# Kernel tuning notes

Measured on AMD Instinct MI355X. Metric: run time of the kernel, lower is better.

The kernel has to match this reference:

```python
import jax, jax.numpy as jnp
import numpy as np

R = 40            # guided-filter radius (81x81 window)
EPS = 1e-3
BETA = 2.996 / 300.0  # visibility_m = 300.0


def _box_sum(x, r=R):
    """Zero-padded sliding-window sum over an (B,C,H,W) tensor.
    Matches F.avg_pool2d(x, 2r+1, stride=1, padding=r) * (2r+1)^2
    (count_include_pad=True), computed in O(HW) via prefix sums."""
    B, C, H, W = x.shape

    def _along(y, axis, L):
        cs = jnp.cumsum(y, axis=axis)
        pad = [(0, 0)] * 4
        pad[axis] = (1, 0)
        cs = jnp.pad(cs, pad)  # cs[i] = sum of first i elements
        hi = jnp.clip(jnp.arange(L) + r + 1, 0, L)
        lo = jnp.clip(jnp.arange(L) - r, 0, L)
        return jnp.take(cs, hi, axis=axis) - jnp.take(cs, lo, axis=axis)

    x = _along(x, 2, H)
    x = _along(x, 3, W)
    return x


def _guided_filter(I, p, r=R, eps=EPS):
    N = (2 * r + 1) ** 2
    mean_I = _box_sum(I, r) / N
    mean_p = _box_sum(p, r) / N
    mean_Ip = _box_sum(I * p, r) / N
    cov_Ip = mean_Ip - mean_I * mean_p
    mean_II = _box_sum(I * I, r) / N
    var_I = mean_II - mean_I * mean_I
    a = cov_Ip / (var_I + eps)
    b = mean_p - a * mean_I
    mean_a = _box_sum(a, r) / N
    mean_b = _box_sum(b, r) / N
    return mean_a * I + mean_b


def setup_inputs() -> dict:
    key = jax.random.key(0)
    k1, k2 = jax.random.split(key)
    B, H, W = 8, 768, 1280
    img = jax.random.uniform(k1, (B, 3, H, W), dtype=jnp.float32)
    depth = jax.random.uniform(k2, (B, 1, H, W), dtype=jnp.float32) * 500.0
    return {"img": img, "depth": depth}


def reference(img, depth):
    B, _, H, W = img.shape
    t_raw = jnp.clip(jnp.exp(-BETA * depth), 0.0, 1.0)          # (B,1,H,W)
    gray = (0.299 * img[:, 0:1] + 0.587 * img[:, 1:2]
            + 0.114 * img[:, 2:3])                               # (B,1,H,W)
    t = _guided_filter(gray, t_raw)                               # (B,1,H,W)

    # atmospheric light A: mean color over the k farthest pixels, per image
    k = max(10, int(0.001 * H * W))
    k = min(k, H * W)
    depth_flat = depth.reshape(B, -1)                             # (B,HW)
    img_flat = img.reshape(B, 3, -1)                              # (B,3,HW)
    _, idx = jax.lax.top_k(depth_flat, k)                         # (B,k)
    A = jnp.take_along_axis(img_flat, idx[:, None, :], axis=2).mean(axis=2)
    A = A.reshape(B, 3, 1, 1)

    return img * t + A * (1.0 - t)
```

## Files before the change

kernel.cpp:

```cpp
#include <hip/hip_runtime.h>
#include <hip/hip_fp16.h>
#include <stdint.h>

typedef unsigned int u32;

#define Bn 8
#define Hn 768
#define Wn 1280
#define HWs (Hn*Wn)
#define Rr 40
#define NNinv (1.0f/6561.0f)
#define KTOP 983
#define BETA_C (2.996f/300.0f)
#define EQCAP 4096
#define TK_BPI 480
#define NCH 96
#define SEGV 16
#define NSEGV 48
#define HIMG 4
#define TK1_WAVES 16
#define TW 640
#define CW 680

#define OFF_F     0
#define OFF_AB1   (16*HWs)
#define OFF_AB2   (24*HWs)
#define OFF_CS4f  (32*HWs)
#define OFF_CS2f  (36*HWs)
#define OFF_TAILf (38*HWs)

#define OFFH_FOVF 0
#define OFFH_AB   (4*HWs)
#define CS_N      (HIMG*NCH*Wn)
#define OFFH_CS4  (12*HWs)
#define OFFH_CS2  (OFFH_CS4 + 4*CS_N)
#define OFFH_TAIL (OFFH_CS2 + 2*CS_N)

__device__ __forceinline__ float4 f4add(float4 a, float4 b){ return make_float4(a.x+b.x,a.y+b.y,a.z+b.z,a.w+b.w); }
__device__ __forceinline__ float4 f4sub(float4 a, float4 b){ return make_float4(a.x-b.x,a.y-b.y,a.z-b.z,a.w-b.w); }

__device__ __forceinline__ u32 h2_to_u32(__half2 h){ union { __half2 h; u32 u; } c; c.h = h; return c.u; }
__device__ __forceinline__ __half2 u32_to_h2(u32 u){ union { u32 u; __half2 h; } c; c.u = u; return c.h; }


__global__ __launch_bounds__(256) void gA_kernel(const float* __restrict__ img, const float* __restrict__ depth,
    uint2* __restrict__ F, float4* __restrict__ CS4){
  __shared__ float4 lds[769];
  __shared__ float4 wtot[4];
  int blk = blockIdx.x;
  int xt = blk & 1;
  int t2 = blk >> 1;
  int b = t2 / NCH, ch = t2 % NCH;
  int x0 = xt*TW;
  int cstart = xt ? (TW - Rr) : 0;
  int tid = threadIdx.x;
  int lane = tid & 63, wv = tid >> 6;
  float4 acc[3];
  #pragma unroll
  for (int j = 0; j < 3; ++j) acc[j] = make_float4(0,0,0,0);
  for (int r = 0; r < 8; ++r){
    int y = ch*8 + r;
    const float* ir = img + ((size_t)(b*3+0)*Hn + y)*Wn + cstart;
    const float* ig = img + ((size_t)(b*3+1)*Hn + y)*Wn + cstart;
    const float* ib = img + ((size_t)(b*3+2)*Hn + y)*Wn + cstart;
    const float* dp = depth + ((size_t)b*Hn + y)*Wn + cstart;
    __syncthreads();
    for (int i = tid; i < 768; i += 256){
      if (i < CW){
        float rr = ir[i], g = ig[i], bb = ib[i];
        float I = 0.299f*rr + 0.587f*g + 0.114f*bb;
        float p = expf(-BETA_C*dp[i]);
        p = fminf(fmaxf(p, 0.0f), 1.0f);
        lds[i] = make_float4(I, p, I*p, I*I);
      } else {
        lds[i] = make_float4(0,0,0,0);
      }
    }
    __syncthreads();
    int base = tid*3;
    float4 loc[3]; float4 tsum = make_float4(0,0,0,0);
    #pragma unroll
    for (int j = 0; j < 3; ++j){ loc[j] = lds[base+j]; tsum = f4add(tsum, loc[j]); }
    float4 v = tsum;
    for (int d = 1; d < 64; d <<= 1){
      float4 o; o.x = __shfl_up(v.x, d); o.y = __shfl_up(v.y, d); o.z = __shfl_up(v.z, d); o.w = __shfl_up(v.w, d);
      if (lane >= d) v = f4add(v, o);
    }
    if (lane == 63) wtot[wv] = v;
    __syncthreads();
    float4 ex = f4sub(v, tsum);
    for (int w = 0; w < wv; ++w) ex = f4add(ex, wtot[w]);
    float4 run = ex;
    #pragma unroll
    for (int j = 0; j < 3; ++j){ lds[base+j] = run; run = f4add(run, loc[j]); }
    __syncthreads();
    #pragma unroll
    for (int j = 0; j < 3; ++j){
      int lx = tid + j*256;
      if (lx < TW){
        int gx = x0 + lx;
        int hi = gx + Rr + 1; if (hi > Wn) hi = Wn;
        int lo = gx - Rr;     if (lo < 0)  lo = 0;
        float4 s = f4sub(lds[hi - cstart], lds[lo - cstart]);
        __half2 h01 = __float22half2_rn(make_float2(s.x, s.y));
        __half2 h23 = __float22half2_rn(make_float2(s.z, s.w));
        F[(size_t)b*HWs + (size_t)y*Wn + gx] = make_uint2(h2_to_u32(h01), h2_to_u32(h23));
        float2 f0 = __half22float2(h01), f1 = __half22float2(h23);
        acc[j] = f4add(acc[j], make_float4(f0.x, f0.y, f1.x, f1.y));
      }
    }
  }
  #pragma unroll
  for (int j = 0; j < 3; ++j){
    int lx = tid + j*256;
    if (lx < TW) CS4[((size_t)b*NCH + ch)*Wn + x0 + lx] = acc[j];
  }
}

__global__ __launch_bounds__(256) void vAf_kernel(const uint2* __restrict__ F, const float4* __restrict__ CS,
    u32* __restrict__ AB){
  int gt = blockIdx.x*256 + threadIdx.x;
  int x  = gt % Wn;
  int t2 = gt / Wn;
  int b = t2 % Bn, s = t2 / Bn;
  const uint2* Fb   = F + (size_t)b*HWs;
  const float4* CSb = CS + (size_t)b*NCH*Wn;
  int y0 = s*SEGV;
  int c0 = 2*s - 5; if (c0 < 0) c0 = 0;
  int c1 = 2*s + 5; if (c1 > NCH) c1 = NCH;
  float4 S = make_float4(0,0,0,0);
  for (int c = c0; c < c1; ++c) S = f4add(S, CSb[(size_t)c*Wn + x]);
  u32* ABb = AB + (size_t)b*HWs;
  #pragma unroll 2
  for (int y = y0; y < y0 + SEGV; ++y){
    int ya = y + Rr;
    if (ya < Hn){
      uint2 u = Fb[(size_t)ya*Wn + x];
      float2 f0 = __half22float2(u32_to_h2(u.x)), f1 = __half22float2(u32_to_h2(u.y));
      S.x += f0.x; S.y += f0.y; S.z += f1.x; S.w += f1.y;
    }
    float mI = S.x*NNinv, mp = S.y*NNinv, mIp = S.z*NNinv, mII = S.w*NNinv;
    float var = mII - mI*mI;
    float a  = (mIp - mI*mp) / (var + 1e-3f);
    float bb = mp - a*mI;
    ABb[(size_t)y*Wn + x] = h2_to_u32(__float22half2_rn(make_float2(a, bb)));
    int yb = y - Rr;
    if (yb >= 0){
      uint2 u = Fb[(size_t)yb*Wn + x];
      float2 f0 = __half22float2(u32_to_h2(u.x)), f1 = __half22float2(u32_to_h2(u.y));
      S.x -= f0.x; S.y -= f0.y; S.z -= f1.x; S.w -= f1.y;
    }
  }
}

__global__ __launch_bounds__(256) void gB_kernel(const u32* __restrict__ AB1, u32* __restrict__ AB2,
    float2* __restrict__ CS2){
  __shared__ float2 lds[769];
  __shared__ float2 wtot[4];
  int blk = blockIdx.x;
  int xt = blk & 1;
  int t2 = blk >> 1;
  int b = t2 / NCH, ch = t2 % NCH;
  int x0 = xt*TW;
  int cstart = xt ? (TW - Rr) : 0;
  int tid = threadIdx.x;
  int lane = tid & 63, wv = tid >> 6;
  float2 acc[3];
  #pragma unroll
  for (int j = 0; j < 3; ++j) acc[j] = make_float2(0,0);
  for (int r = 0; r < 8; ++r){
    int y = ch*8 + r;
    const u32* row = AB1 + (size_t)b*HWs + (size_t)y*Wn + cstart;
    __syncthreads();
    for (int i = tid; i < 768; i += 256){
      if (i < CW) lds[i] = __half22float2(u32_to_h2(row[i]));
      else        lds[i] = make_float2(0,0);
    }
    __syncthreads();
    int base = tid*3;
    float2 loc[3]; float2 tsum = make_float2(0,0);
    #pragma unroll
    for (int j = 0; j < 3; ++j){ loc[j] = lds[base+j]; tsum.x += loc[j].x; tsum.y += loc[j].y; }
    float2 v = tsum;
    for (int d = 1; d < 64; d <<= 1){
      float2 o; o.x = __shfl_up(v.x, d); o.y = __shfl_up(v.y, d);
      if (lane >= d){ v.x += o.x; v.y += o.y; }
    }
    if (lane == 63) wtot[wv] = v;
    __syncthreads();
    float2 ex = make_float2(v.x - tsum.x, v.y - tsum.y);
    for (int w = 0; w < wv; ++w){ ex.x += wtot[w].x; ex.y += wtot[w].y; }
    float2 run = ex;
    #pragma unroll
    for (int j = 0; j < 3; ++j){ lds[base+j] = run; run.x += loc[j].x; run.y += loc[j].y; }
    __syncthreads();
    #pragma unroll
    for (int j = 0; j < 3; ++j){
      int lx = tid + j*256;
      if (lx < TW){
        int gx = x0 + lx;
        int hi = gx + Rr + 1; if (hi > Wn) hi = Wn;
        int lo = gx - Rr;     if (lo < 0)  lo = 0;
        float2 s = make_float2(lds[hi - cstart].x - lds[lo - cstart].x,
                               lds[hi - cstart].y - lds[lo - cstart].y);
        __half2 h = __float22half2_rn(s);
        AB2[(size_t)b*HWs + (size_t)y*Wn + gx] = h2_to_u32(h);
        float2 fr = __half22float2(h);
        acc[j].x += fr.x; acc[j].y += fr.y;
      }
    }
  }
  #pragma unroll
  for (int j = 0; j < 3; ++j){
    int lx = tid + j*256;
    if (lx < TW) CS2[((size_t)b*NCH + ch)*Wn + x0 + lx] = acc[j];
  }
}

__global__ __launch_bounds__(256) void vBf_kernel(const u32* __restrict__ AB2, const float2* __restrict__ CS,
    const float* __restrict__ img, const float* __restrict__ Avec, float* __restrict__ out){
  int gt = blockIdx.x*256 + threadIdx.x;
  int x  = gt % Wn;
  int t2 = gt / Wn;
  int b = t2 % Bn, s = t2 / Bn;
  const u32* ABb = AB2 + (size_t)b*HWs;
  const float2* CSb = CS + (size_t)b*NCH*Wn;
  int y0 = s*SEGV;
  int c0 = 2*s - 5; if (c0 < 0) c0 = 0;
  int c1 = 2*s + 5; if (c1 > NCH) c1 = NCH;
  float2 S = make_float2(0,0);
  for (int c = c0; c < c1; ++c){ float2 t = CSb[(size_t)c*Wn + x]; S.x += t.x; S.y += t.y; }
  float A0 = Avec[b*3+0], A1 = Avec[b*3+1], A2 = Avec[b*3+2];
  const float* ir = img + (size_t)(b*3+0)*HWs;
  const float* ig = img + (size_t)(b*3+1)*HWs;
  const float* ib = img + (size_t)(b*3+2)*HWs;
  float* o0 = out + (size_t)(b*3+0)*HWs;
  float* o1 = out + (size_t)(b*3+1)*HWs;
  float* o2 = out + (size_t)(b*3+2)*HWs;
  #pragma unroll 2
  for (int y = y0; y < y0 + SEGV; ++y){
    int ya = y + Rr;
    if (ya < Hn){ float2 t = __half22float2(u32_to_h2(ABb[(size_t)ya*Wn + x])); S.x += t.x; S.y += t.y; }
    float ma = S.x*NNinv, mb = S.y*NNinv;
    size_t idx = (size_t)y*Wn + x;
    float r = ir[idx], g = ig[idx], bb = ib[idx];
    float gray = 0.299f*r + 0.587f*g + 0.114f*bb;
    float t = ma*gray + mb;
    o0[idx] = r *t + A0*(1.0f - t);
    o1[idx] = g *t + A1*(1.0f - t);
    o2[idx] = bb*t + A2*(1.0f - t);
    int yb = y - Rr;
    if (yb >= 0){ float2 t2v = __half22float2(u32_to_h2(ABb[(size_t)yb*Wn + x])); S.x -= t2v.x; S.y -= t2v.y; }
  }
}


__global__ __launch_bounds__(256) void hA_kernel(const float* __restrict__ img, const float* __restrict__ depth,
    float4* __restrict__ Fd, float4* __restrict__ Fw, int half){
  __shared__ float4 lds[Wn+1];
  __shared__ float4 wtot[4];
  int blk = blockIdx.x;
  int bl = blk / Hn, y = blk % Hn;
  int b = half*HIMG + bl;
  const float* ir = img + ((size_t)(b*3+0)*Hn + y)*Wn;
  const float* ig = img + ((size_t)(b*3+1)*Hn + y)*Wn;
  const float* ib = img + ((size_t)(b*3+2)*Hn + y)*Wn;
  const float* dp = depth + ((size_t)b*Hn + y)*Wn;
  int tid = threadIdx.x;
  for (int i = tid; i < Wn; i += 256){
    float r = ir[i], g = ig[i], bb = ib[i];
    float I = 0.299f*r + 0.587f*g + 0.114f*bb;
    float p = expf(-BETA_C*dp[i]);
    p = fminf(fmaxf(p, 0.0f), 1.0f);
    lds[i] = make_float4(I, p, I*p, I*I);
  }
  __syncthreads();
  float4 loc[5]; float4 tsum = make_float4(0,0,0,0);
  for (int j = 0; j < 5; ++j){ loc[j] = lds[tid*5+j]; tsum = f4add(tsum, loc[j]); }
  int lane = tid & 63, wv = tid >> 6;
  float4 v = tsum;
  for (int d = 1; d < 64; d <<= 1){
    float4 o; o.x = __shfl_up(v.x, d); o.y = __shfl_up(v.y, d); o.z = __shfl_up(v.z, d); o.w = __shfl_up(v.w, d);
    if (lane >= d) v = f4add(v, o);
  }
  if (lane == 63) wtot[wv] = v;
  __syncthreads();
  float4 ex = f4sub(v, tsum);
  for (int w = 0; w < wv; ++w) ex = f4add(ex, wtot[w]);
  float4 run = ex;
  for (int j = 0; j < 5; ++j){ lds[tid*5+j] = run; run = f4add(run, loc[j]); }
  if (tid == 255) lds[Wn] = run;
  __syncthreads();
  float4* F = (bl < 3) ? (Fd + (size_t)bl*HWs) : Fw;
  for (int j = 0; j < 5; ++j){
    int xx = tid + j*256;
    int hi = xx + Rr + 1; if (hi > Wn) hi = Wn;
    int lo = xx - Rr;     if (lo < 0)  lo = 0;
    F[(size_t)y*Wn + xx] = f4sub(lds[hi], lds[lo]);
  }
}

__global__ __launch_bounds__(256) void cs4_kernel(const float4* __restrict__ Fd, const float4* __restrict__ Fw,
    float4* __restrict__ CS){
  int gt = blockIdx.x*256 + threadIdx.x;
  int x  = gt % Wn;
  int t2 = gt / Wn;
  int bl = t2 % HIMG, ch = t2 / HIMG;
  const float4* F = (bl < 3) ? (Fd + (size_t)bl*HWs) : Fw;
  const float4* p = F + (size_t)ch*8*Wn + x;
  float4 s = make_float4(0,0,0,0);
  #pragma unroll
  for (int i = 0; i < 8; ++i) s = f4add(s, p[(size_t)i*Wn]);
  CS[((size_t)bl*NCH + ch)*Wn + x] = s;
}

__global__ __launch_bounds__(256) void vA_kernel(const float4* __restrict__ Fd, const float4* __restrict__ Fw,
    const float4* __restrict__ CS, float2* __restrict__ AB){
  int gt = blockIdx.x*256 + threadIdx.x;
  int x  = gt % Wn;
  int t2 = gt / Wn;
  int bl = t2 % HIMG, s = t2 / HIMG;
  const float4* F   = (bl < 3) ? (Fd + (size_t)bl*HWs) : Fw;
  const float4* CSb = CS + (size_t)bl*NCH*Wn;
  int y0 = s*SEGV;
  int c0 = 2*s - 5; if (c0 < 0) c0 = 0;
  int c1 = 2*s + 5; if (c1 > NCH) c1 = NCH;
  float4 S = make_float4(0,0,0,0);
  for (int c = c0; c < c1; ++c) S = f4add(S, CSb[(size_t)c*Wn + x]);
  float2* ABb = AB + (size_t)bl*HWs;
  #pragma unroll 2
  for (int y = y0; y < y0 + SEGV; ++y){
    int ya = y + Rr;
    if (ya < Hn) S = f4add(S, F[(size_t)ya*Wn + x]);
    float mI = S.x*NNinv, mp = S.y*NNinv, mIp = S.z*NNinv, mII = S.w*NNinv;
    float var = mII - mI*mI;
    float a  = (mIp - mI*mp) / (var + 1e-3f);
    float bb = mp - a*mI;
    ABb[(size_t)y*Wn + x] = make_float2(a, bb);
    int yb = y - Rr;
    if (yb >= 0) S = f4sub(S, F[(size_t)yb*Wn + x]);
  }
}

__global__ __launch_bounds__(256) void hB_kernel(float2* __restrict__ AB){
  __shared__ float2 lds[Wn+1];
  __shared__ float2 wtot[4];
  int blk = blockIdx.x;
  int bl = blk / Hn, y = blk % Hn;
  float2* row = AB + ((size_t)bl*Hn + y)*Wn;
  int tid = threadIdx.x;
  for (int i = tid; i < Wn; i += 256) lds[i] = row[i];
  __syncthreads();
  float2 loc[5]; float2 tsum = make_float2(0,0);
  for (int j = 0; j < 5; ++j){ loc[j] = lds[tid*5+j]; tsum.x += loc[j].x; tsum.y += loc[j].y; }
  int lane = tid & 63, wv = tid >> 6;
  float2 v = tsum;
  for (int d = 1; d < 64; d <<= 1){
    float2 o; o.x = __shfl_up(v.x, d); o.y = __shfl_up(v.y, d);
    if (lane >= d){ v.x += o.x; v.y += o.y; }
  }
  if (lane == 63) wtot[wv] = v;
  __syncthreads();
  float2 ex = make_float2(v.x - tsum.x, v.y - tsum.y);
  for (int w = 0; w < wv; ++w){ ex.x += wtot[w].x; ex.y += wtot[w].y; }
  float2 run = ex;
  for (int j = 0; j < 5; ++j){ lds[tid*5+j] = run; run.x += loc[j].x; run.y += loc[j].y; }
  if (tid == 255) lds[Wn] = run;
  __syncthreads();
  for (int j = 0; j < 5; ++j){
    int xx = tid + j*256;
    int hi = xx + Rr + 1; if (hi > Wn) hi = Wn;
    int lo = xx - Rr;     if (lo < 0)  lo = 0;
    row[xx] = make_float2(lds[hi].x - lds[lo].x, lds[hi].y - lds[lo].y);
  }
}

__global__ __launch_bounds__(256) void cs2_kernel(const float2* __restrict__ AB, float2* __restrict__ CS){
  int gt = blockIdx.x*256 + threadIdx.x;
  int x  = gt % Wn;
  int t2 = gt / Wn;
  int bl = t2 % HIMG, ch = t2 / HIMG;
  const float2* p = AB + (size_t)bl*HWs + (size_t)ch*8*Wn + x;
  float2 s = make_float2(0,0);
  #pragma unroll
  for (int i = 0; i < 8; ++i){ s.x += p[(size_t)i*Wn].x; s.y += p[(size_t)i*Wn].y; }
  CS[((size_t)bl*NCH + ch)*Wn + x] = s;
}

__global__ __launch_bounds__(256) void vB_kernel(const float2* __restrict__ AB, const float2* __restrict__ CS,
    const float* __restrict__ img, const float* __restrict__ Avec, float* __restrict__ out, int half){
  int gt = blockIdx.x*256 + threadIdx.x;
  int x  = gt % Wn;
  int t2 = gt / Wn;
  int bl = t2 % HIMG, s = t2 / HIMG;
  int b = half*HIMG + bl;
  const float2* ABb = AB + (size_t)bl*HWs;
  const float2* CSb = CS + (size_t)bl*NCH*Wn;
  int y0 = s*SEGV;
  int c0 = 2*s - 5; if (c0 < 0) c0 = 0;
  int c1 = 2*s + 5; if (c1 > NCH) c1 = NCH;
  float2 S = make_float2(0,0);
  for (int c = c0; c < c1; ++c){ float2 t = CSb[(size_t)c*Wn + x]; S.x += t.x; S.y += t.y; }
  float A0 = Avec[b*3+0], A1 = Avec[b*3+1], A2 = Avec[b*3+2];
  const float* ir = img + (size_t)(b*3+0)*HWs;
  const float* ig = img + (size_t)(b*3+1)*HWs;
  const float* ib = img + (size_t)(b*3+2)*HWs;
  float* o0 = out + (size_t)(b*3+0)*HWs;
  float* o1 = out + (size_t)(b*3+1)*HWs;
  float* o2 = out + (size_t)(b*3+2)*HWs;
  #pragma unroll 2
  for (int y = y0; y < y0 + SEGV; ++y){
    int ya = y + Rr;
    if (ya < Hn){ float2 t = ABb[(size_t)ya*Wn + x]; S.x += t.x; S.y += t.y; }
    float ma = S.x*NNinv, mb = S.y*NNinv;
    size_t idx = (size_t)y*Wn + x;
    float r = ir[idx], g = ig[idx], bb = ib[idx];
    float gray = 0.299f*r + 0.587f*g + 0.114f*bb;
    float t = ma*gray + mb;
    o0[idx] = r *t + A0*(1.0f - t);
    o1[idx] = g *t + A1*(1.0f - t);
    o2[idx] = bb*t + A2*(1.0f - t);
    int yb = y - Rr;
    if (yb >= 0){ float2 t2v = ABb[(size_t)yb*Wn + x]; S.x -= t2v.x; S.y -= t2v.y; }
  }
}


__global__ __launch_bounds__(1024) void tk1_kernel(const float* __restrict__ depth, u32* __restrict__ hist1){
  __shared__ u32 lh[TK1_WAVES*2048];
  int tid = threadIdx.x;
  for (int i = tid; i < TK1_WAVES*2048; i += 1024) lh[i] = 0;
  __syncthreads();
  int b = blockIdx.x >> 5;
  int slice = blockIdx.x & 31;
  const int per = HWs/32;
  int start = b*HWs + slice*per;
  u32* h = &lh[(tid >> 6) * 2048];
  const float2* dp = (const float2*)(depth + start);
  for (int i = tid; i < per/2; i += 1024){
    float2 v = dp[i];
    u32 u0 = __float_as_uint(v.x), u1 = __float_as_uint(v.y);
    u32 b0 = u0 >> 20, b1 = u1 >> 20;
    atomicAdd(&h[b0 >> 1], (b0 & 1u) ? 65536u : 1u);
    atomicAdd(&h[b1 >> 1], (b1 & 1u) ? 65536u : 1u);
  }
  __syncthreads();
  for (int i = tid; i < 4096; i += 1024){
    u32 s = 0;
    for (int w = 0; w < TK1_WAVES; ++w) s += (lh[w*2048 + (i>>1)] >> ((i&1)*16)) & 0xFFFFu;
    if (s) atomicAdd(&hist1[b*4096+i], s);
  }
}

__global__ __launch_bounds__(256) void tk2_kernel(const u32* __restrict__ hist1,
    u32* __restrict__ selP1, u32* __restrict__ selK1){
  int b = blockIdx.x, tid = threadIdx.x;
  const u32* h = hist1 + b*4096;
  u32 cs = 0; int bb = tid*16;
  for (int i = 0; i < 16; ++i) cs += h[bb+i];
  __shared__ u32 sums[256];
  sums[tid] = cs; __syncthreads();
  u32 above = 0;
  for (int t = tid+1; t < 256; ++t) above += sums[t];
  if (above < KTOP && above + cs >= KTOP){
    u32 acc = above;
    for (int i = 15; i >= 0; --i){
      u32 c = h[bb+i]; acc += c;
      if (acc >= KTOP){ selP1[b] = (u32)(bb+i); selK1[b] = KTOP - (acc - c); break; }
    }
  }
}

__global__ __launch_bounds__(256) void tk3_kernel(const float* __restrict__ depth,
    const u32* __restrict__ selP1, u32* __restrict__ hist2){
  int idx = blockIdx.x*2048 + threadIdx.x;
  int b = blockIdx.x / TK_BPI;
  u32 p1 = selP1[b];
  for (int it = 0; it < 8; ++it, idx += 256){
    u32 u = __float_as_uint(depth[idx]);
    if ((u>>20) == p1) atomicAdd(&hist2[b*65536 + ((u>>4)&0xFFFFu)], 1u);
  }
}

__global__ __launch_bounds__(256) void tk4_kernel(const u32* __restrict__ hist2, const u32* __restrict__ selP1,
    const u32* __restrict__ selK1, u32* __restrict__ selTau, u32* __restrict__ selK2){
  int b = blockIdx.x, tid = threadIdx.x;
  const u32* h = hist2 + b*65536;
  u32 kk = selK1[b];
  u32 cs = 0; int bb = tid*256;
  for (int i = 0; i < 256; ++i) cs += h[bb+i];
  __shared__ u32 sums[256];
  sums[tid] = cs; __syncthreads();
  u32 above = 0;
  for (int t = tid+1; t < 256; ++t) above += sums[t];
  if (above < kk && above + cs >= kk){
    u32 acc = above;
    for (int i = 255; i >= 0; --i){
      u32 c = h[bb+i]; acc += c;
      if (acc >= kk){ selTau[b] = (selP1[b]<<16) | (u32)(bb+i); selK2[b] = kk - (acc - c); break; }
    }
  }
}

__global__ __launch_bounds__(256) void tk5_kernel(const float* __restrict__ depth, const float* __restrict__ img,
    const u32* __restrict__ selTau, u32* __restrict__ eqCount, u32* __restrict__ eqVal, u32* __restrict__ eqIdx,
    float* __restrict__ partial){
  int blk = blockIdx.x;
  int b = blk / TK_BPI;
  u32 tau = selTau[b];
  int idx = blk*2048 + threadIdx.x;
  float cr = 0.f, cg = 0.f, cb = 0.f;
  for (int it = 0; it < 8; ++it, idx += 256){
    int pix = idx - b*HWs;
    u32 u = __float_as_uint(depth[idx]);
    u32 u28 = u >> 4;
    if (u28 > tau){
      cr += img[(size_t)(b*3+0)*HWs + pix];
      cg += img[(size_t)(b*3+1)*HWs + pix];
      cb += img[(size_t)(b*3+2)*HWs + pix];
    } else if (u28 == tau){
      u32 p = atomicAdd(&eqCount[b], 1u);
      if (p < EQCAP){ eqVal[b*EQCAP+p] = u; eqIdx[b*EQCAP+p] = (u32)pix; }
    }
  }
  for (int d = 32; d; d >>= 1){
    cr += __shfl_down(cr, d); cg += __shfl_down(cg, d); cb += __shfl_down(cb, d);
  }
  __shared__ float wsum[4][3];
  int lane = threadIdx.x & 63, wv = threadIdx.x >> 6;
  if (lane == 0){ wsum[wv][0] = cr; wsum[wv][1] = cg; wsum[wv][2] = cb; }
  __syncthreads();
  if (threadIdx.x == 0){
    float r = 0.f, g = 0.f, bl = 0.f;
    for (int w = 0; w < 4; ++w){ r += wsum[w][0]; g += wsum[w][1]; bl += wsum[w][2]; }
    partial[blk*3+0] = r; partial[blk*3+1] = g; partial[blk*3+2] = bl;
  }
}

__global__ void tk6_kernel(const float* __restrict__ img, const u32* __restrict__ eqCount,
    u32* __restrict__ eqVal, const u32* __restrict__ eqIdx, const u32* __restrict__ selK2,
    const float* __restrict__ partial, float* __restrict__ Avec){
  int b = blockIdx.x;
  int tid = threadIdx.x;
  float r = 0.f, g = 0.f, bl = 0.f;
  for (int i = tid; i < TK_BPI; i += 64){
    r  += partial[(b*TK_BPI+i)*3+0];
    g  += partial[(b*TK_BPI+i)*3+1];
    bl += partial[(b*TK_BPI+i)*3+2];
  }
  for (int d = 32; d; d >>= 1){
    r += __shfl_down(r, d); g += __shfl_down(g, d); bl += __shfl_down(bl, d);
  }
  if (tid != 0) return;
  u32 m = eqCount[b]; if (m > EQCAP) m = EQCAP;
  u32 need = selK2[b]; if (need > m) need = m;
  float cr = r, cg = g, cb = bl;
  for (u32 it = 0; it < need; ++it){
    int best = -1; u32 bv = 0, bi = 0;
    for (u32 j = 0; j < m; ++j){
      u32 vv = eqVal[b*EQCAP+j];
      if (vv == 0xFFFFFFFFu) continue;
      u32 ix = eqIdx[b*EQCAP+j];
      if (best < 0 || vv > bv || (vv == bv && ix < bi)){ best = (int)j; bv = vv; bi = ix; }
    }
    eqVal[b*EQCAP+best] = 0xFFFFFFFFu;
    cr += img[(size_t)(b*3+0)*HWs + bi];
    cg += img[(size_t)(b*3+1)*HWs + bi];
    cb += img[(size_t)(b*3+2)*HWs + bi];
  }
  float inv = 1.0f/(float)KTOP;
  Avec[b*3+0] = cr*inv; Avec[b*3+1] = cg*inv; Avec[b*3+2] = cb*inv;
}


extern "C" void kernel_launch(void* const* d_in, const int* in_sizes, int n_in,
                              void* d_out, int out_size, void* d_ws, size_t ws_size,
                              hipStream_t stream){
  const float* img   = (const float*)d_in[0];
  const float* depth = (const float*)d_in[1];
  float* out = (float*)d_out;
  float* ws  = (float*)d_ws;

  const size_t tailFloats = (size_t)Bn*4096 + (size_t)Bn*65536 + 5*Bn
                          + 2*(size_t)Bn*EQCAP + (size_t)Bn*TK_BPI*3 + Bn*3 + 16;
  const size_t needFull = ((size_t)38*HWs + tailFloats) * sizeof(float);
  bool full = (ws_size >= needFull);

  size_t offTail = full ? (size_t)OFF_TAILf : (size_t)OFFH_TAIL;
  u32* tail    = (u32*)(ws + offTail);
  u32* hist1   = tail;
  u32* hist2   = hist1 + Bn*4096;
  u32* selP1   = hist2 + (size_t)Bn*65536;
  u32* selK1   = selP1 + Bn;
  u32* selTau  = selK1 + Bn;
  u32* selK2   = selTau + Bn;
  u32* eqCount = selK2 + Bn;
  u32* eqVal   = eqCount + Bn;
  u32* eqIdx   = eqVal + (size_t)Bn*EQCAP;
  float* partial = (float*)(eqIdx + (size_t)Bn*EQCAP);
  float* Avec    = partial + (size_t)Bn*TK_BPI*3;
  size_t tailBytes = (size_t)((char*)(Avec + Bn*3) - (char*)tail);

  hipMemsetAsync(tail, 0, tailBytes, stream);

  tk1_kernel<<<dim3(Bn*32), dim3(1024), 0, stream>>>(depth, hist1);
  tk2_kernel<<<dim3(Bn),    dim3(256), 0, stream>>>(hist1, selP1, selK1);
  tk3_kernel<<<dim3(Bn*TK_BPI), dim3(256), 0, stream>>>(depth, selP1, hist2);
  tk4_kernel<<<dim3(Bn),    dim3(256), 0, stream>>>(hist2, selP1, selK1, selTau, selK2);
  tk5_kernel<<<dim3(Bn*TK_BPI), dim3(256), 0, stream>>>(depth, img, selTau, eqCount, eqVal, eqIdx, partial);
  tk6_kernel<<<dim3(Bn),    dim3(64),  0, stream>>>(img, eqCount, eqVal, eqIdx, selK2, partial, Avec);

  if (full){
    uint2*  F   = (uint2*)(ws + OFF_F);
    u32*    AB1 = (u32*)(ws + OFF_AB1);
    u32*    AB2 = (u32*)(ws + OFF_AB2);
    float4* CS4 = (float4*)(ws + OFF_CS4f);
    float2* CS2 = (float2*)(ws + OFF_CS2f);
    gA_kernel <<<dim3(Bn*NCH*2),            dim3(256), 0, stream>>>(img, depth, F, CS4);
    vAf_kernel<<<dim3((Bn*Wn*NSEGV)/256),   dim3(256), 0, stream>>>(F, CS4, AB1);
    gB_kernel <<<dim3(Bn*NCH*2),            dim3(256), 0, stream>>>(AB1, AB2, CS2);
    vBf_kernel<<<dim3((Bn*Wn*NSEGV)/256),   dim3(256), 0, stream>>>(AB2, CS2, img, Avec, out);
  } else {
    float4* Fw  = (float4*)(ws + OFFH_FOVF);
    float2* AB  = (float2*)(ws + OFFH_AB);
    float4* CS4 = (float4*)(ws + OFFH_CS4);
    float2* CS2 = (float2*)(ws + OFFH_CS2);
    for (int half = 0; half < 2; ++half){
      float4* Fd = (float4*)out + (size_t)half*3*HWs;
      hA_kernel <<<dim3(HIMG*Hn),            dim3(256), 0, stream>>>(img, depth, Fd, Fw, half);
      cs4_kernel<<<dim3((HIMG*NCH*Wn)/256),  dim3(256), 0, stream>>>(Fd, Fw, CS4);
      vA_kernel <<<dim3((HIMG*Wn*NSEGV)/256),dim3(256), 0, stream>>>(Fd, Fw, CS4, AB);
      hB_kernel <<<dim3(HIMG*Hn),            dim3(256), 0, stream>>>(AB);
      cs2_kernel<<<dim3((HIMG*NCH*Wn)/256),  dim3(256), 0, stream>>>(AB, CS2);
      vB_kernel <<<dim3((HIMG*Wn*NSEGV)/256),dim3(256), 0, stream>>>(AB, CS2, img, Avec, out, half);
    }
  }
}
```

Before: 232.0 us.

## Process two rows per barrier round in row-scan kernels; replace memset with narrow fill kernel

The horizontal prefix-sum kernels gA and gB now stage two rows at once in double-sized shared memory. This halves the number of block-wide barriers per chunk and lets the two rows' wave scans interleave. Separately, the workspace layout is reordered so that only the histograms and the equal-count array need zeroing, and a small fill kernel does that instead of a hipMemsetAsync over the whole tail. The trade-off is higher shared-memory and register use per block, which could lower occupancy.

```diff
diff --git a/kernel.cpp b/kernel.cpp
--- a/kernel.cpp
+++ b/kernel.cpp
@@ -36,17 +36,25 @@
 #define OFFH_CS2  (OFFH_CS4 + 4*CS_N)
 #define OFFH_TAIL (OFFH_CS2 + 2*CS_N)
 
+#define ZERO_U32  (Bn*4096 + Bn*65536 + Bn)
+#define ZERO_U4   (ZERO_U32/4)
+
 __device__ __forceinline__ float4 f4add(float4 a, float4 b){ return make_float4(a.x+b.x,a.y+b.y,a.z+b.z,a.w+b.w); }
 __device__ __forceinline__ float4 f4sub(float4 a, float4 b){ return make_float4(a.x-b.x,a.y-b.y,a.z-b.z,a.w-b.w); }
 
 __device__ __forceinline__ u32 h2_to_u32(__half2 h){ union { __half2 h; u32 u; } c; c.h = h; return c.u; }
 __device__ __forceinline__ __half2 u32_to_h2(u32 u){ union { u32 u; __half2 h; } c; c.u = u; return c.h; }
 
+__global__ __launch_bounds__(256) void fill0_kernel(uint4* __restrict__ p){
+  int i = blockIdx.x*256 + threadIdx.x;
+  if (i < ZERO_U4) p[i] = make_uint4(0,0,0,0);
+}
+
 
 __global__ __launch_bounds__(256) void gA_kernel(const float* __restrict__ img, const float* __restrict__ depth,
     uint2* __restrict__ F, float4* __restrict__ CS4){
-  __shared__ float4 lds[769];
-  __shared__ float4 wtot[4];
+  __shared__ float4 lds[2][769];
+  __shared__ float4 wtot[2][4];
   int blk = blockIdx.x;
   int xt = blk & 1;
   int t2 = blk >> 1;
@@ -58,55 +66,70 @@
   float4 acc[3];
   #pragma unroll
   for (int j = 0; j < 3; ++j) acc[j] = make_float4(0,0,0,0);
-  for (int r = 0; r < 8; ++r){
-    int y = ch*8 + r;
-    const float* ir = img + ((size_t)(b*3+0)*Hn + y)*Wn + cstart;
-    const float* ig = img + ((size_t)(b*3+1)*Hn + y)*Wn + cstart;
-    const float* ib = img + ((size_t)(b*3+2)*Hn + y)*Wn + cstart;
-    const float* dp = depth + ((size_t)b*Hn + y)*Wn + cstart;
-    __syncthreads();
-    for (int i = tid; i < 768; i += 256){
-      if (i < CW){
-        float rr = ir[i], g = ig[i], bb = ib[i];
-        float I = 0.299f*rr + 0.587f*g + 0.114f*bb;
-        float p = expf(-BETA_C*dp[i]);
-        p = fminf(fmaxf(p, 0.0f), 1.0f);
-        lds[i] = make_float4(I, p, I*p, I*I);
-      } else {
-        lds[i] = make_float4(0,0,0,0);
+  for (int rp = 0; rp < 4; ++rp){
+    __syncthreads();
+    #pragma unroll
+    for (int h = 0; h < 2; ++h){
+      int y = ch*8 + rp*2 + h;
+      const float* ir = img + ((size_t)(b*3+0)*Hn + y)*Wn + cstart;
+      const float* ig = img + ((size_t)(b*3+1)*Hn + y)*Wn + cstart;
+      const float* ib = img + ((size_t)(b*3+2)*Hn + y)*Wn + cstart;
+      const float* dp = depth + ((size_t)b*Hn + y)*Wn + cstart;
+      for (int i = tid; i < 768; i += 256){
+        if (i < CW){
+          float rr = ir[i], g = ig[i], bb = ib[i];
+          float I = 0.299f*rr + 0.587f*g + 0.114f*bb;
+          float p = expf(-BETA_C*dp[i]);
+          p = fminf(fmaxf(p, 0.0f), 1.0f);
+          lds[h][i] = make_float4(I, p, I*p, I*I);
+        } else {
+          lds[h][i] = make_float4(0,0,0,0);
+        }
       }
     }
     __syncthreads();
     int base = tid*3;
-    float4 loc[3]; float4 tsum = make_float4(0,0,0,0);
-    #pragma unroll
-    for (int j = 0; j < 3; ++j){ loc[j] = lds[base+j]; tsum = f4add(tsum, loc[j]); }
-    float4 v = tsum;
-    for (int d = 1; d < 64; d <<= 1){
-      float4 o; o.x = __shfl_up(v.x, d); o.y = __shfl_up(v.y, d); o.z = __shfl_up(v.z, d); o.w = __shfl_up(v.w, d);
-      if (lane >= d) v = f4add(v, o);
-    }
-    if (lane == 63) wtot[wv] = v;
-    __syncthreads();
-    float4 ex = f4sub(v, tsum);
-    for (int w = 0; w < wv; ++w) ex = f4add(ex, wtot[w]);
-    float4 run = ex;
-    #pragma unroll
-    for (int j = 0; j < 3; ++j){ lds[base+j] = run; run = f4add(run, loc[j]); }
-    __syncthreads();
-    #pragma unroll
-    for (int j = 0; j < 3; ++j){
-      int lx = tid + j*256;
-      if (lx < TW){
-        int gx = x0 + lx;
-        int hi = gx + Rr + 1; if (hi > Wn) hi = Wn;
-        int lo = gx - Rr;     if (lo < 0)  lo = 0;
-        float4 s = f4sub(lds[hi - cstart], lds[lo - cstart]);
-        __half2 h01 = __float22half2_rn(make_float2(s.x, s.y));
-        __half2 h23 = __float22half2_rn(make_float2(s.z, s.w));
-        F[(size_t)b*HWs + (size_t)y*Wn + gx] = make_uint2(h2_to_u32(h01), h2_to_u32(h23));
-        float2 f0 = __half22float2(h01), f1 = __half22float2(h23);
-        acc[j] = f4add(acc[j], make_float4(f0.x, f0.y, f1.x, f1.y));
+    float4 loc[2][3], vv[2], ts[2];
+    #pragma unroll
+    for (int h = 0; h < 2; ++h){
+      float4 tsum = make_float4(0,0,0,0);
+      #pragma unroll
+      for (int j = 0; j < 3; ++j){ loc[h][j] = lds[h][base+j]; tsum = f4add(tsum, loc[h][j]); }
+      float4 v = tsum;
+      for (int d = 1; d < 64; d <<= 1){
+        float4 o; o.x = __shfl_up(v.x, d); o.y = __shfl_up(v.y, d); o.z = __shfl_up(v.z, d); o.w = __shfl_up(v.w, d);
+        if (lane >= d) v = f4add(v, o);
+      }
+      vv[h] = v; ts[h] = tsum;
+      if (lane == 63) wtot[h][wv] = v;
+    }
+    __syncthreads();
+    #pragma unroll
+    for (int h = 0; h < 2; ++h){
+      float4 ex = f4sub(vv[h], ts[h]);
+      for (int w = 0; w < wv; ++w) ex = f4add(ex, wtot[h][w]);
+      float4 run = ex;
+      #pragma unroll
+      for (int j = 0; j < 3; ++j){ lds[h][base+j] = run; run = f4add(run, loc[h][j]); }
+    }
+    __syncthreads();
+    #pragma unroll
+    for (int h = 0; h < 2; ++h){
+      int y = ch*8 + rp*2 + h;
+      #pragma unroll
+      for (int j = 0; j < 3; ++j){
+        int lx = tid + j*256;
+        if (lx < TW){
+          int gx = x0 + lx;
+          int hi = gx + Rr + 1; if (hi > Wn) hi = Wn;
+          int lo = gx - Rr;     if (lo < 0)  lo = 0;
+          float4 s = f4sub(lds[h][hi - cstart], lds[h][lo - cstart]);
+          __half2 h01 = __float22half2_rn(make_float2(s.x, s.y));
+          __half2 h23 = __float22half2_rn(make_float2(s.z, s.w));
+          F[(size_t)b*HWs + (size_t)y*Wn + gx] = make_uint2(h2_to_u32(h01), h2_to_u32(h23));
+          float2 f0 = __half22float2(h01), f1 = __half22float2(h23);
+          acc[j] = f4add(acc[j], make_float4(f0.x, f0.y, f1.x, f1.y));
+        }
       }
     }
   }
@@ -155,8 +178,8 @@
 
 __global__ __launch_bounds__(256) void gB_kernel(const u32* __restrict__ AB1, u32* __restrict__ AB2,
     float2* __restrict__ CS2){
-  __shared__ float2 lds[769];
-  __shared__ float2 wtot[4];
+  __shared__ float2 lds[2][769];
+  __shared__ float2 wtot[2][4];
   int blk = blockIdx.x;
   int xt = blk & 1;
   int t2 = blk >> 1;
@@ -168,45 +191,60 @@
   float2 acc[3];
   #pragma unroll
   for (int j = 0; j < 3; ++j) acc[j] = make_float2(0,0);
-  for (int r = 0; r < 8; ++r){
-    int y = ch*8 + r;
-    const u32* row = AB1 + (size_t)b*HWs + (size_t)y*Wn + cstart;
-    __syncthreads();
-    for (int i = tid; i < 768; i += 256){
-      if (i < CW) lds[i] = __half22float2(u32_to_h2(row[i]));
-      else        lds[i] = make_float2(0,0);
+  for (int rp = 0; rp < 4; ++rp){
+    __syncthreads();
+    #pragma unroll
+    for (int h = 0; h < 2; ++h){
+      int y = ch*8 + rp*2 + h;
+      const u32* row = AB1 + (size_t)b*HWs + (size_t)y*Wn + cstart;
+      for (int i = tid; i < 768; i += 256){
+        if (i < CW) lds[h][i] = __half22float2(u32_to_h2(row[i]));
+        else        lds[h][i] = make_float2(0,0);
+      }
     }
     __syncthreads();
     int base = tid*3;
-    float2 loc[3]; float2 tsum = make_float2(0,0);
-    #pragma unroll
-    for (int j = 0; j < 3; ++j){ loc[j] = lds[base+j]; tsum.x += loc[j].x; tsum.y += loc[j].y; }
-    float2 v = tsum;
-    for (int d = 1; d < 64; d <<= 1){
-      float2 o; o.x = __shfl_up(v.x, d); o.y = __shfl_up(v.y, d);
-      if (lane >= d){ v.x += o.x; v.y += o.y; }
-    }
-    if (lane == 63) wtot[wv] = v;
-    __syncthreads();
-    float2 ex = make_float2(v.x - tsum.x, v.y - tsum.y);
-    for (int w = 0; w < wv; ++w){ ex.x += wtot[w].x; ex.y += wtot[w].y; }
-    float2 run = ex;
-    #pragma unroll
-    for (int j = 0; j < 3; ++j){ lds[base+j] = run; run.x += loc[j].x; run.y += loc[j].y; }
-    __syncthreads();
-    #pragma unroll
-    for (int j = 0; j < 3; ++j){
-      int lx = tid + j*256;
-      if (lx < TW){
-        int gx = x0 + lx;
-        int hi = gx + Rr + 1; if (hi > Wn) hi = Wn;
-        int lo = gx - Rr;     if (lo < 0)  lo = 0;
-        float2 s = make_float2(lds[hi - cstart].x - lds[lo - cstart].x,
-                               lds[hi - cstart].y - lds[lo - cstart].y);
-        __half2 h = __float22half2_rn(s);
-        AB2[(size_t)b*HWs + (size_t)y*Wn + gx] = h2_to_u32(h);
-        float2 fr = __half22float2(h);
-        acc[j].x += fr.x; acc[j].y += fr.y;
+    float2 loc[2][3], vv[2], ts[2];
+    #pragma unroll
+    for (int h = 0; h < 2; ++h){
+      float2 tsum = make_float2(0,0);
+      #pragma unroll
+      for (int j = 0; j < 3; ++j){ loc[h][j] = lds[h][base+j]; tsum.x += loc[h][j].x; tsum.y += loc[h][j].y; }
+      float2 v = tsum;
+      for (int d = 1; d < 64; d <<= 1){
+        float2 o; o.x = __shfl_up(v.x, d); o.y = __shfl_up(v.y, d);
+        if (lane >= d){ v.x += o.x; v.y += o.y; }
+      }
+      vv[h] = v; ts[h] = tsum;
+      if (lane == 63) wtot[h][wv] = v;
+    }
+    __syncthreads();
+    #pragma unroll
+    for (int h = 0; h < 2; ++h){
+      float2 ex = make_float2(vv[h].x - ts[h].x, vv[h].y - ts[h].y);
+      for (int w = 0; w < wv; ++w){ ex.x += wtot[h][w].x; ex.y += wtot[h][w].y; }
+      float2 run = ex;
+      #pragma unroll
+      for (int j = 0; j < 3; ++j){ lds[h][base+j] = run; run.x += loc[h][j].x; run.y += loc[h][j].y; }
+    }
+    __syncthreads();
+    #pragma unroll
+    for (int h = 0; h < 2; ++h){
+      int y = ch*8 + rp*2 + h;
+      #pragma unroll
+      for (int j = 0; j < 3; ++j){
+        int lx = tid + j*256;
+        if (lx < TW){
+          int gx = x0 + lx;
+          int hi = gx + Rr + 1; if (hi > Wn) hi = Wn;
+          int lo = gx - Rr;     if (lo < 0)  lo = 0;
+          float2 s = make_float2(lds[h][hi - cstart].x - lds[h][lo - cstart].x,
+                                 lds[h][hi - cstart].y - lds[h][lo - cstart].y);
+          __half2 hh = __float22half2_rn(s);
+          AB2[(size_t)b*HWs + (size_t)y*Wn + gx] = h2_to_u32(hh);
+          float2 fr = __half22float2(hh);
+          acc[j].x += fr.x; acc[j].y += fr.y;
+        }
       }
     }
   }
@@ -581,8 +619,8 @@
   float* out = (float*)d_out;
   float* ws  = (float*)d_ws;
 
-  const size_t tailFloats = (size_t)Bn*4096 + (size_t)Bn*65536 + 5*Bn
-                          + 2*(size_t)Bn*EQCAP + (size_t)Bn*TK_BPI*3 + Bn*3 + 16;
+  const size_t tailFloats = (size_t)ZERO_U32 + 4*Bn + 2*(size_t)Bn*EQCAP
+                          + (size_t)Bn*TK_BPI*3 + Bn*3 + 16;
   const size_t needFull = ((size_t)38*HWs + tailFloats) * sizeof(float);
   bool full = (ws_size >= needFull);
 
@@ -590,18 +628,17 @@
   u32* tail    = (u32*)(ws + offTail);
   u32* hist1   = tail;
   u32* hist2   = hist1 + Bn*4096;
-  u32* selP1   = hist2 + (size_t)Bn*65536;
+  u32* eqCount = hist2 + (size_t)Bn*65536;
+  u32* selP1   = eqCount + Bn;
   u32* selK1   = selP1 + Bn;
   u32* selTau  = selK1 + Bn;
   u32* selK2   = selTau + Bn;
-  u32* eqCount = selK2 + Bn;
-  u32* eqVal   = eqCount + Bn;
+  u32* eqVal   = selK2 + Bn;
   u32* eqIdx   = eqVal + (size_t)Bn*EQCAP;
   float* partial = (float*)(eqIdx + (size_t)Bn*EQCAP);
   float* Avec    = partial + (size_t)Bn*TK_BPI*3;
-  size_t tailBytes = (size_t)((char*)(Avec + Bn*3) - (char*)tail);
-
-  hipMemsetAsync(tail, 0, tailBytes, stream);
+
+  fill0_kernel<<<dim3((ZERO_U4 + 255)/256), dim3(256), 0, stream>>>((uint4*)tail);
 
   tk1_kernel<<<dim3(Bn*32), dim3(1024), 0, stream>>>(depth, hist1);
   tk2_kernel<<<dim3(Bn),    dim3(256), 0, stream>>>(hist1, selP1, selK1);
```

After: 242.3 us. 4.4% more time.
